# Kernel tuning notes

Measured on AMD Instinct MI355X. Metric: run time of the kernel, lower is better.

## Reference

```python
import jax, jax.numpy as jnp
import numpy as np

B, C, G, P, W, H = 16, 64, 256, 4096, 1024, 256
WQ = W // 4  # wsi_dim // 4 = 256
D = C + G + WQ  # concat dim fed to score MLP = 576


def _init_linear(key, fan_in, fan_out):
    k1, k2 = jax.random.split(key)
    bound = 1.0 / np.sqrt(fan_in)
    w = jax.random.uniform(k1, (fan_in, fan_out), jnp.float32, -bound, bound)
    b = jax.random.uniform(k2, (fan_out,), jnp.float32, -bound, bound)
    return w, b


def setup_inputs() -> dict:
    key = jax.random.key(0)
    ks = jax.random.split(key, 8)
    cx = jax.random.normal(ks[0], (B, C), jnp.float32)
    gx = jax.random.normal(ks[1], (B, G), jnp.float32)
    wx = jax.random.normal(ks[2], (B, P, W), jnp.float32)
    Wc, bc = _init_linear(ks[3], C, C)        # fc_c
    Wg, bg = _init_linear(ks[4], G, G)        # fc_g
    Ww, bw = _init_linear(ks[5], W, WQ)       # fc_w
    W1, b1 = _init_linear(ks[6], D, H)        # FCLayers hidden
    W2, b2 = _init_linear(ks[7], H, 1)        # FCLayers out
    return {"cx": cx, "gx": gx, "wx": wx,
            "Wc": Wc, "bc": bc, "Wg": Wg, "bg": bg, "Ww": Ww, "bw": bw,
            "W1": W1, "b1": b1, "W2": W2, "b2": b2}


def reference(cx, gx, wx, Wc, bc, Wg, bg, Ww, bw, W1, b1, W2, b2):
    # Per-modality projections
    c = cx @ Wc + bc                      # [B, C]
    g = gx @ Wg + bg                      # [B, G]
    w = jnp.einsum('bpw,wq->bpq', wx, Ww) + bw  # [B, P, WQ]
    # Score MLP on concat(c, g, w_i) for every patch, vectorized by
    # splitting W1 rows over the concat blocks (avoids materializing concat):
    W1c, W1g, W1w = W1[:C], W1[C:C + G], W1[C + G:]
    h = jax.nn.relu((c @ W1c + g @ W1g + b1)[:, None, :]
                    + jnp.einsum('bpq,qh->bph', w, W1w))  # [B, P, H]
    scores = h @ W2 + b2                  # [B, P, 1]
    attn = jax.nn.softmax(scores, axis=1)  # softmax over patches
    return jnp.sum(attn * w, axis=1)      # [B, WQ]
```

## Files before the change

### kernel.cpp

```cpp
#include <hip/hip_runtime.h>
#include <hip/hip_bf16.h>

#define B_   16
#define C_   64
#define G_   256
#define P_   4096
#define W_   1024
#define H_   256
#define WQ_  256
#define M_   (B_ * P_)

typedef __attribute__((ext_vector_type(8))) _Float16 f16x8;
typedef __attribute__((ext_vector_type(4))) float    f32x4;

__device__ __forceinline__ float h2f(ushort u) {
    union { ushort u; _Float16 h; } cv; cv.u = u;
    return (float)cv.h;
}

#define GLOAD16(gsrc, ldst)                                                  \
    __builtin_amdgcn_global_load_lds(                                        \
        (const __attribute__((address_space(1))) unsigned int*)(gsrc),       \
        (__attribute__((address_space(3))) unsigned int*)(ldst), 16, 0, 0)

__device__ __forceinline__ int inv_swz64(int o) {
    const int b8 = (o >> 8) & 1, b7 = (o >> 7) & 1, b6 = (o >> 6) & 1;
    const int b5 = (o >> 5) & 1, b4 = (o >> 4) & 1;
    const int l6 = b6 ^ b8, l5 = b5 ^ b7, l4 = b4 ^ l6;
    return (o & ~0x70) | (l6 << 6) | (l5 << 5) | (l4 << 4);
}

__device__ __forceinline__ void convT_dev(
    const float* __restrict__ src, ushort* __restrict__ dst,
    int K, int N, int blk, float* tile )
{
    const int nb = N >> 6;
    const int k0 = (blk / nb) * 64;
    const int n0 = (blk % nb) * 64;
    const int t = threadIdx.x;
    #pragma unroll
    for (int i = 0; i < 16; ++i) {
        int e = i * 256 + t;
        int kr = e >> 6, nc = e & 63;
        tile[nc * 65 + kr] = src[(size_t)(k0 + kr) * N + n0 + nc];
    }
    __syncthreads();
    #pragma unroll
    for (int i = 0; i < 16; ++i) {
        int e = i * 256 + t;
        int nc = e >> 6, kr = e & 63;
        union { _Float16 h; ushort u; } cv;
        cv.h = (_Float16)tile[nc * 65 + kr];
        dst[(size_t)(n0 + nc) * K + k0 + kr] = cv.u;
    }
}

__global__ __launch_bounds__(256) void setup_kernel(
    const float* __restrict__ Ww,  ushort* __restrict__ WwT,
    const float* __restrict__ W1w, ushort* __restrict__ W1T,
    const float* __restrict__ cx, const float* __restrict__ gx,
    const float* __restrict__ Wc, const float* __restrict__ bc,
    const float* __restrict__ Wg, const float* __restrict__ bg,
    const float* __restrict__ W1, const float* __restrict__ b1,
    float* __restrict__ base_out)
{
    __shared__ float smem[64 * 65];
    const int blk = blockIdx.x;
    if (blk < 64) {
        convT_dev(Ww, WwT, W_, WQ_, blk, smem);
        return;
    }
    if (blk < 80) {
        convT_dev(W1w, W1T, H_, H_, blk - 64, smem);
        return;
    }
    const int b = blk - 80;
    const int t = threadIdx.x;
    float* cxl = smem;
    float* gxl = smem + 64;
    float* cl  = smem + 320;
    float* gl  = smem + 384;

    if (t < C_) cxl[t] = cx[b * C_ + t];
    gxl[t] = gx[b * G_ + t];
    __syncthreads();

    if (t < C_) {
        float acc = bc[t];
        #pragma unroll 4
        for (int i = 0; i < C_; ++i) acc += cxl[i] * Wc[i * C_ + t];
        cl[t] = acc;
    }
    {
        float acc = bg[t];
        #pragma unroll 4
        for (int i = 0; i < G_; ++i) acc += gxl[i] * Wg[i * G_ + t];
        gl[t] = acc;
    }
    __syncthreads();

    float acc = b1[t];
    #pragma unroll 4
    for (int i = 0; i < C_; ++i) acc += cl[i] * W1[i * H_ + t];
    #pragma unroll 4
    for (int i = 0; i < G_; ++i) acc += gl[i] * W1[(C_ + i) * H_ + t];
    base_out[b * H_ + t] = acc;
}

__global__ __launch_bounds__(512, 2) void gemm_w_mfma(
    const float* __restrict__ A,
    const ushort* __restrict__ BT,
    const float* __restrict__ bw,
    ushort* __restrict__ Cout)
{
    __shared__ __align__(16) char smem[65536];
    float*  Af = (float*)smem;
    ushort* Bh = (ushort*)(smem + 32768);

    const int t = threadIdx.x;
    const int row0 = blockIdx.x * 128;
    const int lane = t & 63, wave = t >> 6;
    const int wm = wave >> 2, wn = wave & 3;
    const int l15 = lane & 15, lq = lane >> 4;

    const float *srcA0, *srcA1, *srcA2, *srcA3;
    char *dstA0, *dstA1, *dstA2, *dstA3;
    {
        const int o0 = t * 16, o1 = o0 + 8192, o2 = o0 + 16384, o3 = o0 + 24576;
        const int r0 = o0 >> 8, r1 = o1 >> 8, r2 = o2 >> 8, r3 = o3 >> 8;
        srcA0 = A + (size_t)(row0 + r0) * W_ + (((o0 & 255) ^ ((r0 & 7) << 4)) >> 2);
        srcA1 = A + (size_t)(row0 + r1) * W_ + (((o1 & 255) ^ ((r1 & 7) << 4)) >> 2);
        srcA2 = A + (size_t)(row0 + r2) * W_ + (((o2 & 255) ^ ((r2 & 7) << 4)) >> 2);
        srcA3 = A + (size_t)(row0 + r3) * W_ + (((o3 & 255) ^ ((r3 & 7) << 4)) >> 2);
        dstA0 = (char*)Af + o0; dstA1 = (char*)Af + o1;
        dstA2 = (char*)Af + o2; dstA3 = (char*)Af + o3;
    }
    const ushort *srcB0, *srcB1, *srcB2, *srcB3;
    char *dstB0, *dstB1, *dstB2, *dstB3;
    {
        const int o0 = t * 16, o1 = o0 + 8192, o2 = o0 + 16384, o3 = o0 + 24576;
        const int c0 = o0 >> 7, c1 = o1 >> 7, c2 = o2 >> 7, c3 = o3 >> 7;
        srcB0 = BT + (size_t)c0 * W_ + (((o0 & 127) ^ ((c0 & 7) << 4)) >> 1);
        srcB1 = BT + (size_t)c1 * W_ + (((o1 & 127) ^ ((c1 & 7) << 4)) >> 1);
        srcB2 = BT + (size_t)c2 * W_ + (((o2 & 127) ^ ((c2 & 7) << 4)) >> 1);
        srcB3 = BT + (size_t)c3 * W_ + (((o3 & 127) ^ ((c3 & 7) << 4)) >> 1);
        dstB0 = (char*)Bh + o0; dstB1 = (char*)Bh + o1;
        dstB2 = (char*)Bh + o2; dstB3 = (char*)Bh + o3;
    }

    f32x4 acc[4][4];
    #pragma unroll
    for (int m = 0; m < 4; ++m)
        #pragma unroll
        for (int n = 0; n < 4; ++n) acc[m][n] = (f32x4){0.f, 0.f, 0.f, 0.f};

    for (int k0 = 0; k0 < W_; k0 += 64) {
        if (k0) __syncthreads();
        GLOAD16(srcA0 + k0, dstA0);
        GLOAD16(srcA1 + k0, dstA1);
        GLOAD16(srcA2 + k0, dstA2);
        GLOAD16(srcA3 + k0, dstA3);
        GLOAD16(srcB0 + k0, dstB0);
        GLOAD16(srcB1 + k0, dstB1);
        GLOAD16(srcB2 + k0, dstB2);
        GLOAD16(srcB3 + k0, dstB3);
        __syncthreads();

        #pragma unroll
        for (int ks = 0; ks < 2; ++ks) {
            f16x8 af[4], bf[4];
            #pragma unroll
            for (int m = 0; m < 4; ++m) {
                const int r = wm * 64 + m * 16 + l15;
                const int base = r * 256 + ks * 128 + lq * 32;
                const int swz  = (r & 7) << 4;
                const f32x4 a0 = *(const f32x4*)((const char*)Af + (base ^ swz));
                const f32x4 a1 = *(const f32x4*)((const char*)Af + ((base + 16) ^ swz));
                f16x8 h;
                h[0] = (_Float16)a0[0]; h[1] = (_Float16)a0[1];
                h[2] = (_Float16)a0[2]; h[3] = (_Float16)a0[3];
                h[4] = (_Float16)a1[0]; h[5] = (_Float16)a1[1];
                h[6] = (_Float16)a1[2]; h[7] = (_Float16)a1[3];
                af[m] = h;
            }
            #pragma unroll
            for (int n = 0; n < 4; ++n) {
                const int c = wn * 64 + n * 16 + l15;
                const int byte = (c * 128 + ks * 64 + lq * 16) ^ ((c & 7) << 4);
                bf[n] = *(const f16x8*)((const char*)Bh + byte);
            }
            #pragma unroll
            for (int m = 0; m < 4; ++m)
                #pragma unroll
                for (int n = 0; n < 4; ++n)
                    acc[m][n] = __builtin_amdgcn_mfma_f32_16x16x32_f16(
                        af[m], bf[n], acc[m][n], 0, 0, 0);
        }
    }

    float bwv[4];
    #pragma unroll
    for (int n = 0; n < 4; ++n) bwv[n] = bw[wn * 64 + n * 16 + l15];
    #pragma unroll
    for (int m = 0; m < 4; ++m)
        #pragma unroll
        for (int reg = 0; reg < 4; ++reg) {
            const size_t r = (size_t)row0 + wm * 64 + m * 16 + lq * 4 + reg;
            #pragma unroll
            for (int n = 0; n < 4; ++n) {
                union { _Float16 h; ushort u; } cv;
                cv.h = (_Float16)(acc[m][n][reg] + bwv[n]);
                Cout[r * WQ_ + wn * 64 + n * 16 + l15] = cv.u;
            }
        }
}

__global__ __launch_bounds__(512) void gemm_scores_mfma(
    const ushort* __restrict__ A16,
    const ushort* __restrict__ BT,
    const float* __restrict__ base_,
    const float* __restrict__ W2,
    const float* __restrict__ b2,
    float* __restrict__ scores)
{
    __shared__ __align__(16) ushort Ah[128 * 32];
    __shared__ __align__(16) ushort Bh[256 * 32];
    __shared__ float red[4][128];
    const int t = threadIdx.x;
    const int row0 = blockIdx.x * 128;
    const int b = blockIdx.x >> 5;
    const int lane = t & 63, wave = t >> 6;
    const int wm = wave >> 2, wn = wave & 3;
    const int l15 = lane & 15, lq = lane >> 4;

    const int oA = t * 16;
    const int lA = inv_swz64(oA);
    const ushort* srcA = A16 + (size_t)(row0 + (lA >> 6)) * H_ + ((lA & 63) >> 1);
    char* dstA = (char*)Ah + oA;

    const int oB0 = t * 16, oB1 = t * 16 + 8192;
    const int lB0 = inv_swz64(oB0), lB1 = inv_swz64(oB1);
    const ushort* srcB0 = BT + (size_t)(lB0 >> 6) * H_ + ((lB0 & 63) >> 1);
    const ushort* srcB1 = BT + (size_t)(lB1 >> 6) * H_ + ((lB1 & 63) >> 1);
    char* dstB0 = (char*)Bh + oB0;
    char* dstB1 = (char*)Bh + oB1;

    f32x4 acc[4][4];
    #pragma unroll
    for (int m = 0; m < 4; ++m)
        #pragma unroll
        for (int n = 0; n < 4; ++n) acc[m][n] = (f32x4){0.f, 0.f, 0.f, 0.f};

    for (int k0 = 0; k0 < H_; k0 += 32) {
        if (k0) __syncthreads();
        GLOAD16(srcA + k0, dstA);
        GLOAD16(srcB0 + k0, dstB0);
        GLOAD16(srcB1 + k0, dstB1);
        __syncthreads();

        f16x8 af[4], bf[4];
        #pragma unroll
        for (int m = 0; m < 4; ++m) {
            const int r = wm * 64 + m * 16 + l15;
            const int byte = (r * 64 + lq * 16) ^ ((r & 7) << 4);
            af[m] = *(const f16x8*)((const char*)Ah + byte);
        }
        #pragma unroll
        for (int n = 0; n < 4; ++n) {
            const int c = wn * 64 + n * 16 + l15;
            const int byte = (c * 64 + lq * 16) ^ ((c & 7) << 4);
            bf[n] = *(const f16x8*)((const char*)Bh + byte);
        }
        #pragma unroll
        for (int m = 0; m < 4; ++m)
            #pragma unroll
            for (int n = 0; n < 4; ++n)
                acc[m][n] = __builtin_amdgcn_mfma_f32_16x16x32_f16(
                    af[m], bf[n], acc[m][n], 0, 0, 0);
    }

    float basev[4], w2v[4];
    #pragma unroll
    for (int n = 0; n < 4; ++n) {
        const int col = wn * 64 + n * 16 + l15;
        basev[n] = base_[b * H_ + col];
        w2v[n] = W2[col];
    }
    __syncthreads();
    #pragma unroll
    for (int m = 0; m < 4; ++m)
        #pragma unroll
        for (int reg = 0; reg < 4; ++reg) {
            float s = 0.f;
            #pragma unroll
            for (int n = 0; n < 4; ++n) {
                float h = acc[m][n][reg] + basev[n];
                h = fmaxf(h, 0.f);
                s += h * w2v[n];
            }
            s += __shfl_xor(s, 1, 64);
            s += __shfl_xor(s, 2, 64);
            s += __shfl_xor(s, 4, 64);
            s += __shfl_xor(s, 8, 64);
            if (l15 == 0) red[wn][wm * 64 + m * 16 + lq * 4 + reg] = s;
        }
    __syncthreads();
    if (t < 128) {
        scores[row0 + t] = red[0][t] + red[1][t] + red[2][t] + red[3][t] + b2[0];
    }
}

__global__ __launch_bounds__(256) void weighted_partial_kernel(
    const ushort* __restrict__ wmat16, const float* __restrict__ scores,
    float* __restrict__ part)
{
    const int blk = blockIdx.x;
    const int b   = blk >> 5;
    const int sl  = blk & 31;
    const int t   = threadIdx.x;
    const int rg  = t >> 5;
    const int q8  = (t & 31) * 8;
    __shared__ float red[8][WQ_];
    __shared__ float mred[4];

    float mv = -1e30f;
    for (int p = t; p < P_; p += 256) mv = fmaxf(mv, scores[b * P_ + p]);
    #pragma unroll
    for (int d = 1; d < 64; d <<= 1) mv = fmaxf(mv, __shfl_xor(mv, d, 64));
    if ((t & 63) == 0) mred[t >> 6] = mv;
    __syncthreads();
    const float m = fmaxf(fmaxf(mred[0], mred[1]), fmaxf(mred[2], mred[3]));

    float acc[8];
    #pragma unroll
    for (int j = 0; j < 8; ++j) acc[j] = 0.f;

    const int p0 = sl * 128 + rg * 16;
    for (int p = p0; p < p0 + 16; ++p) {
        const float e = expf(scores[b * P_ + p] - m);
        const uint4 raw = *(const uint4*)(wmat16 + ((size_t)b * P_ + p) * WQ_ + q8);
        const ushort* u = (const ushort*)&raw;
        #pragma unroll
        for (int j = 0; j < 8; ++j) acc[j] += e * h2f(u[j]);
    }
    #pragma unroll
    for (int j = 0; j < 8; ++j) red[rg][q8 + j] = acc[j];
    __syncthreads();
    float s = 0.f;
    #pragma unroll
    for (int g = 0; g < 8; ++g) s += red[g][t];
    part[(size_t)(b * 32 + sl) * WQ_ + t] = s;
}

__global__ __launch_bounds__(256) void finalize_kernel(
    const float* __restrict__ part, const float* __restrict__ scores,
    float* __restrict__ out)
{
    const int b = blockIdx.x;
    const int t = threadIdx.x;
    __shared__ float mred[4];
    __shared__ float zred[4];

    float mv = -1e30f;
    for (int p = t; p < P_; p += 256) mv = fmaxf(mv, scores[b * P_ + p]);
    #pragma unroll
    for (int d = 1; d < 64; d <<= 1) mv = fmaxf(mv, __shfl_xor(mv, d, 64));
    if ((t & 63) == 0) mred[t >> 6] = mv;
    __syncthreads();
    const float m = fmaxf(fmaxf(mred[0], mred[1]), fmaxf(mred[2], mred[3]));

    float zv = 0.f;
    for (int p = t; p < P_; p += 256) zv += expf(scores[b * P_ + p] - m);
    #pragma unroll
    for (int d = 1; d < 64; d <<= 1) zv += __shfl_xor(zv, d, 64);
    if ((t & 63) == 0) zred[t >> 6] = zv;
    __syncthreads();
    const float z = zred[0] + zred[1] + zred[2] + zred[3];

    float acc = 0.f;
    #pragma unroll
    for (int sl = 0; sl < 32; ++sl) acc += part[(size_t)(b * 32 + sl) * WQ_ + t];
    out[b * WQ_ + t] = acc / z;
}

extern "C" void kernel_launch(void* const* d_in, const int* in_sizes, int n_in,
                              void* d_out, int out_size, void* d_ws, size_t ws_size,
                              hipStream_t stream) {
    const float* cx = (const float*)d_in[0];
    const float* gx = (const float*)d_in[1];
    const float* wx = (const float*)d_in[2];
    const float* Wc = (const float*)d_in[3];
    const float* bc = (const float*)d_in[4];
    const float* Wg = (const float*)d_in[5];
    const float* bg = (const float*)d_in[6];
    const float* Ww = (const float*)d_in[7];
    const float* bw = (const float*)d_in[8];
    const float* W1 = (const float*)d_in[9];
    const float* b1 = (const float*)d_in[10];
    const float* W2 = (const float*)d_in[11];
    const float* b2 = (const float*)d_in[12];
    float* out = (float*)d_out;

    float* ws        = (float*)d_ws;
    ushort* ws_w16   = (ushort*)ws;
    float* ws_scores = ws + (size_t)M_ * WQ_ / 2;
    float* ws_base   = ws_scores + M_;
    float* ws_part   = ws_base + B_ * H_;
    ushort* WwT16    = (ushort*)(ws_part + B_ * 32 * WQ_);
    ushort* W1T16    = WwT16 + (size_t)W_ * WQ_;

    setup_kernel<<<96, 256, 0, stream>>>(
        Ww, WwT16, W1 + (size_t)(C_ + G_) * H_, W1T16,
        cx, gx, Wc, bc, Wg, bg, W1, b1, ws_base);

    gemm_w_mfma<<<M_ / 128, 512, 0, stream>>>(wx, WwT16, bw, ws_w16);

    gemm_scores_mfma<<<M_ / 128, 512, 0, stream>>>(
        ws_w16, W1T16, ws_base, W2, b2, ws_scores);

    weighted_partial_kernel<<<B_ * 32, 256, 0, stream>>>(ws_w16, ws_scores, ws_part);

    finalize_kernel<<<B_, 256, 0, stream>>>(ws_part, ws_scores, out);
}
```

Measured before the change: 176.8 us.

## Double-buffer the fc_w GEMM K loop with async LDS loads and waitcnt

Restructures the main projection GEMM from a single 64-wide K stage into two 32-wide K stages in LDS. The global-to-LDS loads for step k+2 are issued while step k is being computed, and s_waitcnt vmcnt controls when each buffer is ready. The goal is to hide global memory latency behind the MFMA work. The cost is twice as many barrier rounds, and the code depends on an inv_swz64 helper defined elsewhere and on exact vmcnt counting.

```diff
diff --git a/kernel.cpp b/kernel.cpp
--- a/kernel.cpp
+++ b/kernel.cpp
@@ -114,8 +114,6 @@
     ushort* __restrict__ Cout)
 {
     __shared__ __align__(16) char smem[65536];
-    float*  Af = (float*)smem;
-    ushort* Bh = (ushort*)(smem + 32768);
 
     const int t = threadIdx.x;
     const int row0 = blockIdx.x * 128;
@@ -123,29 +121,25 @@
     const int wm = wave >> 2, wn = wave & 3;
     const int l15 = lane & 15, lq = lane >> 4;
 
-    const float *srcA0, *srcA1, *srcA2, *srcA3;
-    char *dstA0, *dstA1, *dstA2, *dstA3;
-    {
-        const int o0 = t * 16, o1 = o0 + 8192, o2 = o0 + 16384, o3 = o0 + 24576;
-        const int r0 = o0 >> 8, r1 = o1 >> 8, r2 = o2 >> 8, r3 = o3 >> 8;
-        srcA0 = A + (size_t)(row0 + r0) * W_ + (((o0 & 255) ^ ((r0 & 7) << 4)) >> 2);
-        srcA1 = A + (size_t)(row0 + r1) * W_ + (((o1 & 255) ^ ((r1 & 7) << 4)) >> 2);
-        srcA2 = A + (size_t)(row0 + r2) * W_ + (((o2 & 255) ^ ((r2 & 7) << 4)) >> 2);
-        srcA3 = A + (size_t)(row0 + r3) * W_ + (((o3 & 255) ^ ((r3 & 7) << 4)) >> 2);
-        dstA0 = (char*)Af + o0; dstA1 = (char*)Af + o1;
-        dstA2 = (char*)Af + o2; dstA3 = (char*)Af + o3;
-    }
-    const ushort *srcB0, *srcB1, *srcB2, *srcB3;
-    char *dstB0, *dstB1, *dstB2, *dstB3;
-    {
-        const int o0 = t * 16, o1 = o0 + 8192, o2 = o0 + 16384, o3 = o0 + 24576;
-        const int c0 = o0 >> 7, c1 = o1 >> 7, c2 = o2 >> 7, c3 = o3 >> 7;
-        srcB0 = BT + (size_t)c0 * W_ + (((o0 & 127) ^ ((c0 & 7) << 4)) >> 1);
-        srcB1 = BT + (size_t)c1 * W_ + (((o1 & 127) ^ ((c1 & 7) << 4)) >> 1);
-        srcB2 = BT + (size_t)c2 * W_ + (((o2 & 127) ^ ((c2 & 7) << 4)) >> 1);
-        srcB3 = BT + (size_t)c3 * W_ + (((o3 & 127) ^ ((c3 & 7) << 4)) >> 1);
-        dstB0 = (char*)Bh + o0; dstB1 = (char*)Bh + o1;
-        dstB2 = (char*)Bh + o2; dstB3 = (char*)Bh + o3;
+    const int oA0 = t * 16, oA1 = t * 16 + 8192;
+    const int rA0 = oA0 >> 7, rA1 = oA1 >> 7;
+    const float* srcA0 = A + (size_t)(row0 + rA0) * W_
+                           + (((oA0 & 127) ^ ((rA0 & 7) << 4)) >> 2);
+    const float* srcA1 = A + (size_t)(row0 + rA1) * W_
+                           + (((oA1 & 127) ^ ((rA1 & 7) << 4)) >> 2);
+    const int oB0 = t * 16, oB1 = t * 16 + 8192;
+    const int lB0 = inv_swz64(oB0), lB1 = inv_swz64(oB1);
+    const ushort* srcB0 = BT + (size_t)(lB0 >> 6) * W_ + ((lB0 & 63) >> 1);
+    const ushort* srcB1 = BT + (size_t)(lB1 >> 6) * W_ + ((lB1 & 63) >> 1);
+
+#define STAGE_W(BUF, K0)                                                     \
+    {                                                                        \
+        char* ab = smem + (BUF) * 16384;                                     \
+        char* bb = smem + 32768 + (BUF) * 16384;                             \
+        GLOAD16(srcA0 + (K0), ab + oA0);                                     \
+        GLOAD16(srcA1 + (K0), ab + oA1);                                     \
+        GLOAD16(srcB0 + (K0), bb + oB0);                                     \
+        GLOAD16(srcB1 + (K0), bb + oB1);                                     \
     }
 
     f32x4 acc[4][4];
@@ -154,49 +148,51 @@
         #pragma unroll
         for (int n = 0; n < 4; ++n) acc[m][n] = (f32x4){0.f, 0.f, 0.f, 0.f};
 
-    for (int k0 = 0; k0 < W_; k0 += 64) {
-        if (k0) __syncthreads();
-        GLOAD16(srcA0 + k0, dstA0);
-        GLOAD16(srcA1 + k0, dstA1);
-        GLOAD16(srcA2 + k0, dstA2);
-        GLOAD16(srcA3 + k0, dstA3);
-        GLOAD16(srcB0 + k0, dstB0);
-        GLOAD16(srcB1 + k0, dstB1);
-        GLOAD16(srcB2 + k0, dstB2);
-        GLOAD16(srcB3 + k0, dstB3);
-        __syncthreads();
-
-        #pragma unroll
-        for (int ks = 0; ks < 2; ++ks) {
-            f16x8 af[4], bf[4];
+    STAGE_W(0, 0)
+    STAGE_W(1, 32)
+
+    #pragma unroll 1
+    for (int kt = 0; kt < 32; ++kt) {
+        const int cur = kt & 1;
+        if (kt < 31) asm volatile("s_waitcnt vmcnt(4)" ::: "memory");
+        else         asm volatile("s_waitcnt vmcnt(0)" ::: "memory");
+        __builtin_amdgcn_sched_barrier(0);
+        __builtin_amdgcn_s_barrier();
+
+        const char* Af = smem + cur * 16384;
+        const char* Bh = smem + 32768 + cur * 16384;
+        f16x8 af[4], bf[4];
+        #pragma unroll
+        for (int m = 0; m < 4; ++m) {
+            const int r = wm * 64 + m * 16 + l15;
+            const int base = r * 128 + lq * 32;
+            const int swz  = (r & 7) << 4;
+            const f32x4 a0 = *(const f32x4*)(Af + (base ^ swz));
+            const f32x4 a1 = *(const f32x4*)(Af + ((base + 16) ^ swz));
+            f16x8 h;
+            h[0] = (_Float16)a0[0]; h[1] = (_Float16)a0[1];
+            h[2] = (_Float16)a0[2]; h[3] = (_Float16)a0[3];
+            h[4] = (_Float16)a1[0]; h[5] = (_Float16)a1[1];
+            h[6] = (_Float16)a1[2]; h[7] = (_Float16)a1[3];
+            af[m] = h;
+        }
+        #pragma unroll
+        for (int n = 0; n < 4; ++n) {
+            const int c = wn * 64 + n * 16 + l15;
+            bf[n] = *(const f16x8*)(Bh + ((c * 64 + lq * 16) ^ ((c & 7) << 4)));
+        }
+        #pragma unroll
+        for (int m = 0; m < 4; ++m)
             #pragma unroll
-            for (int m = 0; m < 4; ++m) {
-                const int r = wm * 64 + m * 16 + l15;
-                const int base = r * 256 + ks * 128 + lq * 32;
-                const int swz  = (r & 7) << 4;
-                const f32x4 a0 = *(const f32x4*)((const char*)Af + (base ^ swz));
-                const f32x4 a1 = *(const f32x4*)((const char*)Af + ((base + 16) ^ swz));
-                f16x8 h;
-                h[0] = (_Float16)a0[0]; h[1] = (_Float16)a0[1];
-                h[2] = (_Float16)a0[2]; h[3] = (_Float16)a0[3];
-                h[4] = (_Float16)a1[0]; h[5] = (_Float16)a1[1];
-                h[6] = (_Float16)a1[2]; h[7] = (_Float16)a1[3];
-                af[m] = h;
-            }
-            #pragma unroll
-            for (int n = 0; n < 4; ++n) {
-                const int c = wn * 64 + n * 16 + l15;
-                const int byte = (c * 128 + ks * 64 + lq * 16) ^ ((c & 7) << 4);
-                bf[n] = *(const f16x8*)((const char*)Bh + byte);
-            }
-            #pragma unroll
-            for (int m = 0; m < 4; ++m)
-                #pragma unroll
-                for (int n = 0; n < 4; ++n)
-                    acc[m][n] = __builtin_amdgcn_mfma_f32_16x16x32_f16(
-                        af[m], bf[n], acc[m][n], 0, 0, 0);
-        }
-    }
+            for (int n = 0; n < 4; ++n)
+                acc[m][n] = __builtin_amdgcn_mfma_f32_16x16x32_f16(
+                    af[m], bf[n], acc[m][n], 0, 0, 0);
+
+        __builtin_amdgcn_sched_barrier(0);
+        __builtin_amdgcn_s_barrier();
+        if (kt + 2 < 32) STAGE_W(cur, (kt + 2) * 32)
+    }
+#undef STAGE_W
 
     float bwv[4];
     #pragma unroll
```

Measured after the change: 157.8 us. -10.8%, faster.
